# Optimization experiments

Hardware: AMD Instinct MI355X
Metric: run time of the kernel (lower is better)

The kernel has to match this reference:

```python
import jax, jax.numpy as jnp
import numpy as np

B, QT, KVT, M, H = 64, 1, 256, 32, 128

def setup_inputs() -> dict:
    key = jax.random.key(0)
    kq, kk, kv = jax.random.split(key, 3)
    q = jax.random.normal(kq, (B, QT, M * H), dtype=jnp.float32)
    k = jax.random.normal(kk, (B, KVT, M * H), dtype=jnp.float32)
    v = jax.random.normal(kv, (B, KVT, M * H), dtype=jnp.float32)
    return {"q": q, "k": k, "v": v}

def reference(q, k, v):
    # reshape to [B, T, M, H]
    q = q.reshape(B, QT, M, H)
    k = k.reshape(B, KVT, M, H)
    v = v.reshape(B, KVT, M, H)
    # score: [B, M, QT, KVT]  (NOTE: no 1/sqrt(H) scaling, matching source)
    score = jnp.einsum('bqmh,bkmh->bmqk', q, k)
    attn = jax.nn.softmax(score, axis=-1)
    # out: [B, M, QT, H]
    out = jnp.einsum('bmqk,bkmh->bmqh', attn, v)
    return out
```

## Files before the change

kernel.cpp:

```cpp
#include <hip/hip_runtime.h>


constexpr int KVT = 256;
constexpr int M   = 32;
constexpr int H   = 128;
constexpr int MH  = M * H;

__global__ __launch_bounds__(256) void mme_attn_kernel(
    const float* __restrict__ q,
    const float* __restrict__ k,
    const float* __restrict__ v,
    float* __restrict__ out)
{
    __shared__ float  q_s[H];
    __shared__ float  sc[KVT];
    __shared__ float  red[8];
    __shared__ float4 o4[256];

    const int bm  = blockIdx.x;
    const int b   = bm >> 5;
    const int m   = bm & 31;
    const int tid = threadIdx.x;

    const size_t kbase = (size_t)b * KVT * MH + (size_t)m * H;

    if (tid < H) q_s[tid] = q[(size_t)b * MH + (size_t)m * H + tid];
    __syncthreads();

    float s;
    {
        const float4* kp = (const float4*)(k + kbase + (size_t)tid * MH);
        const float4* qp = (const float4*)q_s;
        float acc = 0.f;
#pragma unroll
        for (int i = 0; i < H / 4; ++i) {
            float4 kk = kp[i];
            float4 qq = qp[i];
            acc += kk.x * qq.x + kk.y * qq.y + kk.z * qq.z + kk.w * qq.w;
        }
        s = acc;
    }

    const int lane = tid & 63;
    const int wv   = tid >> 6;

    float mx = s;
#pragma unroll
    for (int off = 32; off > 0; off >>= 1)
        mx = fmaxf(mx, __shfl_xor(mx, off));
    if (lane == 0) red[wv] = mx;
    __syncthreads();
    mx = fmaxf(fmaxf(red[0], red[1]), fmaxf(red[2], red[3]));

    float p = __expf(s - mx);
    float sm = p;
#pragma unroll
    for (int off = 32; off > 0; off >>= 1)
        sm += __shfl_xor(sm, off);
    if (lane == 0) red[4 + wv] = sm;
    __syncthreads();
    sm = (red[4] + red[5]) + (red[6] + red[7]);

    sc[tid] = p * __frcp_rn(sm);
    __syncthreads();

    const int c4  = tid & 31;
    const int seg = tid >> 5;

    float4 acc4 = {0.f, 0.f, 0.f, 0.f};
    const float* vb = v + kbase + (size_t)c4 * 4;
#pragma unroll 4
    for (int t = seg * 32; t < seg * 32 + 32; ++t) {
        float pt  = sc[t];
        float4 vv = *(const float4*)(vb + (size_t)t * MH);
        acc4.x += pt * vv.x;
        acc4.y += pt * vv.y;
        acc4.z += pt * vv.z;
        acc4.w += pt * vv.w;
    }
    o4[tid] = acc4;
    __syncthreads();

    if (tid < 32) {
        float4 r = o4[tid];
#pragma unroll
        for (int sgi = 1; sgi < 8; ++sgi) {
            float4 t4 = o4[sgi * 32 + tid];
            r.x += t4.x; r.y += t4.y; r.z += t4.z; r.w += t4.w;
        }
        ((float4*)(out + (size_t)bm * H))[tid] = r;
    }
}

extern "C" void kernel_launch(void* const* d_in, const int* in_sizes, int n_in,
                              void* d_out, int out_size, void* d_ws, size_t ws_size,
                              hipStream_t stream) {
    const float* q = (const float*)d_in[0];
    const float* k = (const float*)d_in[1];
    const float* v = (const float*)d_in[2];
    float* out = (float*)d_out;

    mme_attn_kernel<<<2048, 256, 0, stream>>>(q, k, v, out);
}
```

Before: 511.5 us.

## Split KV sequence across blocks with contiguous row reads and a combine pass

Replaces the per-(batch, head) kernel with a split-KV scheme. Each block handles one batch and a 16-token slice for all 32 heads, so K and V rows are read as full contiguous 16KB rows instead of strided 512-byte per-head segments. Partial outputs plus per-slice max and sum go to workspace, and a second kernel rescales and combines them. This adds a kernel launch and workspace traffic, and falls back to the old kernel if the workspace is too small.

```diff
diff --git a/kernel.cpp b/kernel.cpp
--- a/kernel.cpp
+++ b/kernel.cpp
@@ -1,32 +1,153 @@
 #include <hip/hip_runtime.h>
 
 
-constexpr int KVT = 256;
-constexpr int M   = 32;
-constexpr int H   = 128;
-constexpr int MH  = M * H;
-
-__global__ __launch_bounds__(256) void mme_attn_kernel(
+constexpr int B    = 64;
+constexpr int KVT  = 256;
+constexpr int Mh   = 32;
+constexpr int H    = 128;
+constexpr int MH   = Mh * H;
+constexpr int MH4  = MH / 4;
+constexpr int SPLIT = 16;
+constexpr int TBLK  = KVT / SPLIT;
+
+__global__ __launch_bounds__(256) void attn_partial(
     const float* __restrict__ q,
     const float* __restrict__ k,
     const float* __restrict__ v,
+    float* __restrict__ outp,
+    float* __restrict__ mxw,
+    float* __restrict__ smw)
+{
+    __shared__ float4 q4s[MH4];
+    __shared__ float  sc[Mh][TBLK];
+
+    const int bid = blockIdx.x;
+    const int b   = bid / SPLIT;
+    const int sp  = bid % SPLIT;
+    const int t0  = sp * TBLK;
+    const int tid = threadIdx.x;
+    const int w    = tid >> 6;
+    const int lane = tid & 63;
+
+    const float4* q4 = (const float4*)q + (size_t)b * MH4;
+#pragma unroll
+    for (int j = 0; j < 4; ++j) q4s[tid + j * 256] = q4[tid + j * 256];
+    __syncthreads();
+
+    const float4* k4 = (const float4*)k + (size_t)(b * KVT + t0) * MH4;
+#pragma unroll 4
+    for (int t = 0; t < TBLK; ++t) {
+        const float4* kr = k4 + (size_t)t * MH4;
+#pragma unroll
+        for (int i = 0; i < 4; ++i) {
+            const int f = w * 256 + i * 64 + lane;
+            float4 kk = kr[f];
+            float4 qq = q4s[f];
+            float d = kk.x * qq.x + kk.y * qq.y + kk.z * qq.z + kk.w * qq.w;
+#pragma unroll
+            for (int off = 16; off; off >>= 1) d += __shfl_xor(d, off);
+            if ((lane & 31) == 0)
+                sc[w * 8 + 2 * i + (lane >> 5)][t] = d;
+        }
+    }
+    __syncthreads();
+
+    {
+        const int g = tid & 7;
+        const int m = tid >> 3;
+        float s0 = sc[m][g], s1 = sc[m][g + 8];
+        float mx = fmaxf(s0, s1);
+#pragma unroll
+        for (int off = 1; off < 8; off <<= 1) mx = fmaxf(mx, __shfl_xor(mx, off));
+        float p0 = __expf(s0 - mx), p1 = __expf(s1 - mx);
+        float ss = p0 + p1;
+#pragma unroll
+        for (int off = 1; off < 8; off <<= 1) ss += __shfl_xor(ss, off);
+        sc[m][g] = p0; sc[m][g + 8] = p1;
+        if (g == 0) {
+            mxw[(size_t)bid * Mh + m] = mx;
+            smw[(size_t)bid * Mh + m] = ss;
+        }
+    }
+    __syncthreads();
+
+    float4 acc[4];
+#pragma unroll
+    for (int i = 0; i < 4; ++i) acc[i] = make_float4(0.f, 0.f, 0.f, 0.f);
+    int mi[4];
+#pragma unroll
+    for (int i = 0; i < 4; ++i) mi[i] = w * 8 + 2 * i + (lane >> 5);
+
+    const float4* v4 = (const float4*)v + (size_t)(b * KVT + t0) * MH4;
+#pragma unroll 4
+    for (int t = 0; t < TBLK; ++t) {
+        const float4* vr = v4 + (size_t)t * MH4;
+#pragma unroll
+        for (int i = 0; i < 4; ++i) {
+            float  p  = sc[mi[i]][t];
+            float4 vv = vr[w * 256 + i * 64 + lane];
+            acc[i].x += p * vv.x; acc[i].y += p * vv.y;
+            acc[i].z += p * vv.z; acc[i].w += p * vv.w;
+        }
+    }
+    float4* op4 = (float4*)outp + (size_t)bid * MH4;
+#pragma unroll
+    for (int i = 0; i < 4; ++i) op4[w * 256 + i * 64 + lane] = acc[i];
+}
+
+__global__ __launch_bounds__(64) void attn_combine(
+    const float* __restrict__ outp,
+    const float* __restrict__ mxw,
+    const float* __restrict__ smw,
     float* __restrict__ out)
+{
+    const int bm  = blockIdx.x;
+    const int b   = bm >> 5;
+    const int m   = bm & 31;
+    const int tid = threadIdx.x;
+
+    float mxs[SPLIT];
+    float mg = -3.0e38f;
+#pragma unroll
+    for (int s = 0; s < SPLIT; ++s) {
+        mxs[s] = mxw[(size_t)(b * SPLIT + s) * Mh + m];
+        mg = fmaxf(mg, mxs[s]);
+    }
+    float wsc[SPLIT];
+    float sg = 0.f;
+#pragma unroll
+    for (int s = 0; s < SPLIT; ++s) {
+        wsc[s] = __expf(mxs[s] - mg);
+        sg += wsc[s] * smw[(size_t)(b * SPLIT + s) * Mh + m];
+    }
+    const float inv = 1.f / sg;
+
+    if (tid < 32) {
+        float4 o = make_float4(0.f, 0.f, 0.f, 0.f);
+#pragma unroll
+        for (int s = 0; s < SPLIT; ++s) {
+            float4 t4 = ((const float4*)outp)[(size_t)(b * SPLIT + s) * MH4 + m * 32 + tid];
+            o.x += wsc[s] * t4.x; o.y += wsc[s] * t4.y;
+            o.z += wsc[s] * t4.z; o.w += wsc[s] * t4.w;
+        }
+        o.x *= inv; o.y *= inv; o.z *= inv; o.w *= inv;
+        ((float4*)out)[(size_t)bm * 32 + tid] = o;
+    }
+}
+
+__global__ __launch_bounds__(256) void mme_attn_fallback(
+    const float* __restrict__ q, const float* __restrict__ k,
+    const float* __restrict__ v, float* __restrict__ out)
 {
     __shared__ float  q_s[H];
     __shared__ float  sc[KVT];
     __shared__ float  red[8];
     __shared__ float4 o4[256];
 
-    const int bm  = blockIdx.x;
-    const int b   = bm >> 5;
-    const int m   = bm & 31;
-    const int tid = threadIdx.x;
-
+    const int bm = blockIdx.x, b = bm >> 5, m = bm & 31, tid = threadIdx.x;
     const size_t kbase = (size_t)b * KVT * MH + (size_t)m * H;
-
     if (tid < H) q_s[tid] = q[(size_t)b * MH + (size_t)m * H + tid];
     __syncthreads();
-
     float s;
     {
         const float4* kp = (const float4*)(k + kbase + (size_t)tid * MH);
@@ -34,53 +155,38 @@
         float acc = 0.f;
 #pragma unroll
         for (int i = 0; i < H / 4; ++i) {
-            float4 kk = kp[i];
-            float4 qq = qp[i];
+            float4 kk = kp[i]; float4 qq = qp[i];
             acc += kk.x * qq.x + kk.y * qq.y + kk.z * qq.z + kk.w * qq.w;
         }
         s = acc;
     }
-
-    const int lane = tid & 63;
-    const int wv   = tid >> 6;
-
+    const int lane = tid & 63, wv = tid >> 6;
     float mx = s;
 #pragma unroll
-    for (int off = 32; off > 0; off >>= 1)
-        mx = fmaxf(mx, __shfl_xor(mx, off));
+    for (int off = 32; off > 0; off >>= 1) mx = fmaxf(mx, __shfl_xor(mx, off));
     if (lane == 0) red[wv] = mx;
     __syncthreads();
     mx = fmaxf(fmaxf(red[0], red[1]), fmaxf(red[2], red[3]));
-
-    float p = __expf(s - mx);
-    float sm = p;
-#pragma unroll
-    for (int off = 32; off > 0; off >>= 1)
-        sm += __shfl_xor(sm, off);
+    float p = __expf(s - mx), sm = p;
+#pragma unroll
+    for (int off = 32; off > 0; off >>= 1) sm += __shfl_xor(sm, off);
     if (lane == 0) red[4 + wv] = sm;
     __syncthreads();
     sm = (red[4] + red[5]) + (red[6] + red[7]);
-
     sc[tid] = p * __frcp_rn(sm);
     __syncthreads();
-
-    const int c4  = tid & 31;
-    const int seg = tid >> 5;
-
+    const int c4 = tid & 31, seg = tid >> 5;
     float4 acc4 = {0.f, 0.f, 0.f, 0.f};
     const float* vb = v + kbase + (size_t)c4 * 4;
 #pragma unroll 4
     for (int t = seg * 32; t < seg * 32 + 32; ++t) {
-        float pt  = sc[t];
+        float pt = sc[t];
         float4 vv = *(const float4*)(vb + (size_t)t * MH);
-        acc4.x += pt * vv.x;
-        acc4.y += pt * vv.y;
-        acc4.z += pt * vv.z;
-        acc4.w += pt * vv.w;
+        acc4.x += pt * vv.x; acc4.y += pt * vv.y;
+        acc4.z += pt * vv.z; acc4.w += pt * vv.w;
     }
     o4[tid] = acc4;
     __syncthreads();
-
     if (tid < 32) {
         float4 r = o4[tid];
 #pragma unroll
@@ -100,5 +206,17 @@
     const float* v = (const float*)d_in[2];
     float* out = (float*)d_out;
 
-    mme_attn_kernel<<<2048, 256, 0, stream>>>(q, k, v, out);
-}
+    const size_t n_outp = (size_t)B * SPLIT * MH;
+    const size_t n_stat = (size_t)B * SPLIT * Mh;
+    const size_t need   = (n_outp + 2 * n_stat) * sizeof(float);
+
+    if (ws_size >= need) {
+        float* outp = (float*)d_ws;
+        float* mxw  = outp + n_outp;
+        float* smw  = mxw + n_stat;
+        attn_partial<<<B * SPLIT, 256, 0, stream>>>(q, k, v, outp, mxw, smw);
+        attn_combine<<<B * Mh, 64, 0, stream>>>(outp, mxw, smw, out);
+    } else {
+        mme_attn_fallback<<<B * Mh, 256, 0, stream>>>(q, k, v, out);
+    }
+}
```

Result: no change. 518.5 us (+1.4%).
